# Kernel optimization log

Measured on AMD Instinct MI355X. Metric: run time of the kernel, lower is better.

The kernel has to match this reference:

```python
import jax, jax.numpy as jnp
import numpy as np

N, NFEAT, NHID, NHEADS, NCLASS = 8192, 512, 64, 8, 40
ALPHA = 0.2
NEG = jnp.float32(-9e15)


def _gat_layer(h, W, a, concat):
    # h: [N, Fin], W: [Fin, Fout], a: [2*Fout, 1]
    Fout = W.shape[1]
    Wh = h @ W                      # [N, Fout]
    f1 = Wh @ a[:Fout]              # [N, 1]
    f2 = Wh @ a[Fout:]              # [N, 1]
    e = jax.nn.leaky_relu(f1 + f2.T, negative_slope=ALPHA)  # [N, N]
    # NOTE: source masks on e > 0 (adj is NOT used) - replicate faithfully
    att = jax.nn.softmax(jnp.where(e > 0, e, NEG), axis=1)
    h_prime = att @ Wh              # [N, Fout]
    return jax.nn.elu(h_prime) if concat else h_prime


def setup_inputs() -> dict:
    key = jax.random.key(0)
    ks = jax.random.split(key, 6)
    x = jax.random.normal(ks[0], (N, NFEAT), dtype=jnp.float32)
    adj = jax.random.randint(ks[1], (N, N), 0, 2).astype(jnp.bool_)  # unused by math, kept for fidelity
    s = 0.1
    W_heads = jax.random.normal(ks[2], (NHEADS, NFEAT, NHID), dtype=jnp.float32) * s
    a_heads = jax.random.normal(ks[3], (NHEADS, 2 * NHID, 1), dtype=jnp.float32) * s
    W_out = jax.random.normal(ks[4], (NHID * NHEADS, NCLASS), dtype=jnp.float32) * s
    a_out = jax.random.normal(ks[5], (2 * NCLASS, 1), dtype=jnp.float32) * s
    return {"x": x, "adj": adj, "W_heads": W_heads, "a_heads": a_heads,
            "W_out": W_out, "a_out": a_out}


def reference(x, adj, W_heads, a_heads, W_out, a_out):
    # multi-head GAT layers (concat=True), vmapped over heads
    heads = jax.vmap(lambda W, a: _gat_layer(x, W, a, True))(W_heads, a_heads)  # [H, N, NHID]
    h = jnp.transpose(heads, (1, 0, 2)).reshape(N, NHEADS * NHID)
    # output attention layer (concat=False), then elu + log_softmax
    out = _gat_layer(h, W_out, a_out, False)
    out = jax.nn.elu(out)
    return jax.nn.log_softmax(out, axis=1)
```

## Files before the change

### kernel.cpp

```cpp
#include <hip/hip_runtime.h>
#include <math.h>

#define N_NODES 8192
#define NFEAT 512
#define NHID 64
#define NHEADS 8
#define NCLASS 40
#define NCHUNK 128
#define CHUNK 64
#define NB 4096

using bf16x8 = __attribute__((ext_vector_type(8))) short;
using f32x4 = __attribute__((ext_vector_type(4))) float;

__device__ __forceinline__ ushort f2b(float f) {
  uint u = __builtin_bit_cast(uint, f);
  u += 0x7FFFu + ((u >> 16) & 1u);
  return (ushort)(u >> 16);
}
__device__ __forceinline__ float b2f(ushort h) {
  uint u = (uint)h << 16;
  return __builtin_bit_cast(float, u);
}
__device__ __forceinline__ uint encf(float f) {
  uint u = __builtin_bit_cast(uint, f);
  return u ^ ((u >> 31) ? 0xFFFFFFFFu : 0x80000000u);
}
__device__ __forceinline__ float decf(uint u) {
  u ^= ((u >> 31) ? 0x80000000u : 0xFFFFFFFFu);
  return __builtin_bit_cast(float, u);
}
__device__ __forceinline__ float3 load_rng(const uint* mm, int head) {
  float h = decf(mm[head * 2]);
  float l = decf(~mm[head * 2 + 1]);
  float scale = (float)NB / fmaxf(h - l, 1e-30f);
  return make_float3(l, scale, h);
}
__device__ __forceinline__ int bucket_of(float v, float lo, float scale) {
  float u = fminf(fmaxf((v - lo) * scale, 0.f), (float)(NB - 1));
  return (int)u;
}

__global__ __launch_bounds__(256) void prep_k(const float* __restrict__ W_heads,
                                              ushort* __restrict__ bth,
                                              ushort* __restrict__ btl,
                                              float* __restrict__ zbase,
                                              int zcount) {
  int gid = blockIdx.x * 256 + threadIdx.x;
  int n = gid >> 9, c = gid & 511;
  int h = n >> 6, f = n & 63;
  float w = W_heads[((size_t)h * NFEAT + c) * NHID + f];
  ushort hh = f2b(w);
  bth[gid] = hh;
  btl[gid] = f2b(w - b2f(hh));
  if (gid < zcount) zbase[gid] = 0.f;
}

__global__ __launch_bounds__(256) void gemm1_k(const float* __restrict__ x,
                                               const ushort* __restrict__ bth,
                                               const ushort* __restrict__ btl,
                                               const float* __restrict__ a_heads,
                                               float* __restrict__ Wh,
                                               float* __restrict__ f1,
                                               float* __restrict__ f2,
                                               float* __restrict__ meanS,
                                               uint* __restrict__ mm1) {
  const int row0 = blockIdx.x * 128, col0 = blockIdx.y * 128;
  const int tid = threadIdx.x;
  const int wave = tid >> 6, lane = tid & 63;
  const int wr = wave >> 1, wc = wave & 1;
  __shared__ ushort Ah[128 * 40], Al[128 * 40], Bh[128 * 40], Bl[128 * 40];
  __shared__ float cs[2][64];
  __shared__ uint lmax[2], lmin[2];
  if (tid < 2) { lmax[tid] = 0u; lmin[tid] = 0u; }
  if (tid < 128) cs[tid >> 6][tid & 63] = 0.f;
  f32x4 acc[4][4] = {};
  const int sr = tid >> 1, sh = (tid & 1) * 16;
  const int fr = lane & 15, quad = lane >> 4;
  for (int k0 = 0; k0 < NFEAT; k0 += 32) {
    {
      const float* xs = x + (size_t)(row0 + sr) * NFEAT + k0 + sh;
      float av[16];
      *reinterpret_cast<float4*>(&av[0])  = *reinterpret_cast<const float4*>(xs);
      *reinterpret_cast<float4*>(&av[4])  = *reinterpret_cast<const float4*>(xs + 4);
      *reinterpret_cast<float4*>(&av[8])  = *reinterpret_cast<const float4*>(xs + 8);
      *reinterpret_cast<float4*>(&av[12]) = *reinterpret_cast<const float4*>(xs + 12);
      uint uh[8], ul[8];
#pragma unroll
      for (int q = 0; q < 8; ++q) {
        ushort h0 = f2b(av[2 * q]), h1 = f2b(av[2 * q + 1]);
        ushort l0 = f2b(av[2 * q] - b2f(h0)), l1 = f2b(av[2 * q + 1] - b2f(h1));
        uh[q] = (uint)h0 | ((uint)h1 << 16);
        ul[q] = (uint)l0 | ((uint)l1 << 16);
      }
      *reinterpret_cast<uint4*>(&Ah[sr * 40 + sh])     = make_uint4(uh[0], uh[1], uh[2], uh[3]);
      *reinterpret_cast<uint4*>(&Ah[sr * 40 + sh + 8]) = make_uint4(uh[4], uh[5], uh[6], uh[7]);
      *reinterpret_cast<uint4*>(&Al[sr * 40 + sh])     = make_uint4(ul[0], ul[1], ul[2], ul[3]);
      *reinterpret_cast<uint4*>(&Al[sr * 40 + sh + 8]) = make_uint4(ul[4], ul[5], ul[6], ul[7]);
      size_t boff = (size_t)(col0 + sr) * NFEAT + k0 + sh;
      *reinterpret_cast<uint4*>(&Bh[sr * 40 + sh])     = *reinterpret_cast<const uint4*>(bth + boff);
      *reinterpret_cast<uint4*>(&Bh[sr * 40 + sh + 8]) = *reinterpret_cast<const uint4*>(bth + boff + 8);
      *reinterpret_cast<uint4*>(&Bl[sr * 40 + sh])     = *reinterpret_cast<const uint4*>(btl + boff);
      *reinterpret_cast<uint4*>(&Bl[sr * 40 + sh + 8]) = *reinterpret_cast<const uint4*>(btl + boff + 8);
    }
    __syncthreads();
    bf16x8 afh[4], afl[4], bfh[4], bfl[4];
#pragma unroll
    for (int q = 0; q < 4; ++q) {
      afh[q] = *reinterpret_cast<const bf16x8*>(&Ah[(wr * 64 + q * 16 + fr) * 40 + quad * 8]);
      afl[q] = *reinterpret_cast<const bf16x8*>(&Al[(wr * 64 + q * 16 + fr) * 40 + quad * 8]);
      bfh[q] = *reinterpret_cast<const bf16x8*>(&Bh[(wc * 64 + q * 16 + fr) * 40 + quad * 8]);
      bfl[q] = *reinterpret_cast<const bf16x8*>(&Bl[(wc * 64 + q * 16 + fr) * 40 + quad * 8]);
    }
#pragma unroll
    for (int qr = 0; qr < 4; ++qr)
#pragma unroll
      for (int qc = 0; qc < 4; ++qc) {
        acc[qr][qc] = __builtin_amdgcn_mfma_f32_16x16x32_bf16(afl[qr], bfh[qc], acc[qr][qc], 0, 0, 0);
        acc[qr][qc] = __builtin_amdgcn_mfma_f32_16x16x32_bf16(afh[qr], bfl[qc], acc[qr][qc], 0, 0, 0);
        acc[qr][qc] = __builtin_amdgcn_mfma_f32_16x16x32_bf16(afh[qr], bfh[qc], acc[qr][qc], 0, 0, 0);
      }
    __syncthreads();
  }
  const int head = blockIdx.y * 2 + wc;
#pragma unroll
  for (int qr = 0; qr < 4; ++qr)
#pragma unroll
    for (int qc = 0; qc < 4; ++qc)
#pragma unroll
      for (int i = 0; i < 4; ++i) {
        int row = row0 + wr * 64 + qr * 16 + quad * 4 + i;
        int col = col0 + wc * 64 + qc * 16 + fr;
        Wh[(size_t)row * NFEAT + col] = acc[qr][qc][i];
      }
  const float* ah = a_heads + head * 2 * NHID;
  float a1v[4], a2v[4];
#pragma unroll
  for (int qc = 0; qc < 4; ++qc) { a1v[qc] = ah[qc * 16 + fr]; a2v[qc] = ah[NHID + qc * 16 + fr]; }
#pragma unroll
  for (int qr = 0; qr < 4; ++qr)
#pragma unroll
    for (int i = 0; i < 4; ++i) {
      float s1 = 0.f, s2 = 0.f;
#pragma unroll
      for (int qc = 0; qc < 4; ++qc) { s1 += acc[qr][qc][i] * a1v[qc]; s2 += acc[qr][qc][i] * a2v[qc]; }
#pragma unroll
      for (int m = 1; m < 16; m <<= 1) { s1 += __shfl_xor(s1, m, 64); s2 += __shfl_xor(s2, m, 64); }
      if (fr == 0) {
        int row = row0 + wr * 64 + qr * 16 + quad * 4 + i;
        f1[(head << 13) + row] = s1;
        f2[(head << 13) + row] = s2;
        atomicMax(&lmax[wc], encf(s2));
        atomicMax(&lmin[wc], ~encf(s2));
      }
    }
#pragma unroll
  for (int qc = 0; qc < 4; ++qc) {
    float v = 0.f;
#pragma unroll
    for (int qr = 0; qr < 4; ++qr)
#pragma unroll
      for (int i = 0; i < 4; ++i) v += acc[qr][qc][i];
    v += __shfl_xor(v, 16, 64);
    v += __shfl_xor(v, 32, 64);
    if (quad == 0) atomicAdd(&cs[wc][qc * 16 + fr], v);
  }
  __syncthreads();
  if (tid < 128) atomicAdd(&meanS[(blockIdx.y * 2 + (tid >> 6)) * NHID + (tid & 63)], cs[tid >> 6][tid & 63]);
  if (tid < 2) {
    atomicMax(&mm1[(blockIdx.y * 2 + tid) * 2], lmax[tid]);
    atomicMax(&mm1[(blockIdx.y * 2 + tid) * 2 + 1], lmin[tid]);
  }
}

__global__ __launch_bounds__(256) void gemm2_k(const float* __restrict__ H,
                                               const float* __restrict__ Wout,
                                               const float* __restrict__ a_out,
                                               float* __restrict__ Wh2,
                                               float* __restrict__ f1b,
                                               float* __restrict__ f2b,
                                               float* __restrict__ meanS2,
                                               uint* __restrict__ mm2) {
  const int row0 = blockIdx.x * 32;
  const int tid = threadIdx.x;
  __shared__ float As[32][33];
  __shared__ float Bs[32][40];
  __shared__ float cs[NCLASS];
  __shared__ uint lmax, lmin;
  if (tid < NCLASS) cs[tid] = 0.f;
  if (tid == 0) { lmax = 0u; lmin = 0u; }
  const int m = tid >> 3;
  const int n0 = (tid & 7) * 5;
  float acc[5] = {};
  for (int k0 = 0; k0 < NFEAT; k0 += 32) {
    {
      int kk = tid & 31, mq = tid >> 5;
#pragma unroll
      for (int r = 0; r < 4; ++r)
        As[kk][mq * 4 + r] = H[(size_t)(row0 + mq * 4 + r) * NFEAT + k0 + kk];
    }
    {
#pragma unroll
      for (int r = 0; r < 5; ++r) {
        int idx = tid + r * 256;
        if (idx < 1280) {
          int c = idx / 40, n = idx - c * 40;
          Bs[c][n] = Wout[(size_t)(k0 + c) * NCLASS + n];
        }
      }
    }
    __syncthreads();
#pragma unroll
    for (int kk = 0; kk < 32; ++kk) {
      float a = As[kk][m];
#pragma unroll
      for (int q = 0; q < 5; ++q) acc[q] += a * Bs[kk][n0 + q];
    }
    __syncthreads();
  }
#pragma unroll
  for (int q = 0; q < 5; ++q) Wh2[(size_t)(row0 + m) * NCLASS + n0 + q] = acc[q];
  float p1 = 0.f, p2 = 0.f;
#pragma unroll
  for (int q = 0; q < 5; ++q) {
    p1 += acc[q] * a_out[n0 + q];
    p2 += acc[q] * a_out[NCLASS + n0 + q];
  }
  p1 += __shfl_xor(p1, 1, 64); p1 += __shfl_xor(p1, 2, 64); p1 += __shfl_xor(p1, 4, 64);
  p2 += __shfl_xor(p2, 1, 64); p2 += __shfl_xor(p2, 2, 64); p2 += __shfl_xor(p2, 4, 64);
  if ((tid & 7) == 0) {
    f1b[row0 + m] = p1;
    f2b[row0 + m] = p2;
    atomicMax(&lmax, encf(p2));
    atomicMax(&lmin, ~encf(p2));
  }
#pragma unroll
  for (int q = 0; q < 5; ++q) atomicAdd(&cs[n0 + q], acc[q]);
  __syncthreads();
  if (tid < NCLASS) atomicAdd(&meanS2[tid], cs[tid]);
  if (tid == 0) { atomicMax(&mm2[0], lmax); atomicMax(&mm2[1], lmin); }
}

__global__ __launch_bounds__(1024) void bucket_k(const float* __restrict__ f2,
                                                 const uint* __restrict__ mm,
                                                 int* __restrict__ bs,
                                                 int* __restrict__ idxs,
                                                 float* __restrict__ f2s,
                                                 float* __restrict__ g) {
  __shared__ int sb[NB];
  const int head = blockIdx.x, tid = threadIdx.x;
  const int base = head * N_NODES;
  float3 rg = load_rng(mm, head);
#pragma unroll
  for (int r = 0; r < NB / 1024; ++r) sb[tid + r * 1024] = 0;
  __syncthreads();
  float v[8];
  int bk[8];
#pragma unroll
  for (int r = 0; r < 8; ++r) {
    v[r] = f2[base + tid + r * 1024];
    bk[r] = bucket_of(v[r], rg.x, rg.y);
    atomicAdd(&sb[bk[r]], 1);
  }
  __syncthreads();
  for (int st = 1; st < NB; st <<= 1) {
    int t[NB / 1024];
#pragma unroll
    for (int r = 0; r < NB / 1024; ++r) { int i = tid + r * 1024; t[r] = (i >= st) ? sb[i - st] : 0; }
    __syncthreads();
#pragma unroll
    for (int r = 0; r < NB / 1024; ++r) sb[tid + r * 1024] += t[r];
    __syncthreads();
  }
  int ex[NB / 1024];
#pragma unroll
  for (int r = 0; r < NB / 1024; ++r) {
    int b = tid + r * 1024;
    ex[r] = b ? sb[b - 1] : 0;
    bs[head * (NB + 1) + b] = ex[r];
  }
  if (tid == 0) bs[head * (NB + 1) + NB] = sb[NB - 1];
  __syncthreads();
#pragma unroll
  for (int r = 0; r < NB / 1024; ++r) sb[tid + r * 1024] = ex[r];
  __syncthreads();
#pragma unroll
  for (int r = 0; r < 8; ++r) {
    int pos = atomicAdd(&sb[bk[r]], 1);
    int i = tid + r * 1024;
    idxs[base + pos] = i;
    f2s[base + pos] = v[r];
    g[base + pos] = expf(v[r] - rg.z);
  }
}

template <int F, int LD, int COLSTEP>
__global__ __launch_bounds__(256) void scanA_k(const float* __restrict__ Wh,
                                               const float* __restrict__ g,
                                               const int* __restrict__ idxs,
                                               float* __restrict__ S,
                                               float* __restrict__ D,
                                               float* __restrict__ T_,
                                               float* __restrict__ Td) {
  constexpr int PAD = (F == 64) ? 66 : 42;
  const int head = blockIdx.y, chunk = blockIdx.x;
  const int tid = threadIdx.x, w = tid >> 6, lane = tid & 63;
  const int base = head << 13;
  const int kbase = base + chunk * CHUNK;
  __shared__ float Sloc[64][PAD];
  __shared__ float Dloc[64];
  __shared__ float wtot[4][PAD];
  __shared__ float wtotD[4];
  int myj = 0; float myg = 0.f;
  if (lane < 16) {
    myj = idxs[kbase + w * 16 + lane];
    myg = g[kbase + w * 16 + lane];
  }
  float acc = 0.f, accD = 0.f;
#pragma unroll
  for (int kk = 15; kk >= 0; --kk) {
    int j = __shfl(myj, kk, 64);
    float gk = __shfl(myg, kk, 64);
    float wv = (lane < F) ? Wh[(size_t)j * LD + head * COLSTEP + lane] : 0.f;
    acc += gk * wv;
    accD += gk;
    if (lane < F) Sloc[w * 16 + kk][lane] = acc;
    if (lane == 0) Dloc[w * 16 + kk] = accD;
  }
  if (lane < F) wtot[w][lane] = acc;
  if (lane == 0) wtotD[w] = accD;
  __syncthreads();
  float off = 0.f, offD = 0.f;
#pragma unroll
  for (int w2 = 1; w2 < 4; ++w2) {
    if (w + w2 < 4) {
      off += (lane < F) ? wtot[w + w2][lane] : 0.f;
      offD += wtotD[w + w2];
    }
  }
#pragma unroll
  for (int kk = 0; kk < 16; ++kk) {
    int e = w * 16 + kk;
    if (lane < F) S[(size_t)(kbase + e) * F + lane] = Sloc[e][lane] + off;
    if (lane == 0) D[kbase + e] = Dloc[e] + offD;
  }
  if (w == 0) {
    if (lane < F) T_[(size_t)(head * NCHUNK + chunk) * F + lane] = wtot[0][lane] + off;
    if (lane == 0) Td[head * NCHUNK + chunk] = wtotD[0] + offD;
  }
}

template <int F>
__global__ __launch_bounds__(1024) void scanB_k(float* __restrict__ T_, float* __restrict__ Td) {
  __shared__ float s[NCHUNK * F];
  __shared__ float td[NCHUNK];
  int head = blockIdx.x;
  int tid = threadIdx.x, slot = tid >> 6, lane = tid & 63;
#pragma unroll
  for (int r = 0; r < 8; ++r) {
    int c = r * 16 + slot;
    if (lane < F) s[c * F + lane] = T_[(size_t)(head * NCHUNK + c) * F + lane];
  }
  if (tid < NCHUNK) td[tid] = Td[head * NCHUNK + tid];
  __syncthreads();
  for (int st = 1; st < NCHUNK; st <<= 1) {
    float v[8];
    float tv = 0.f;
#pragma unroll
    for (int r = 0; r < 8; ++r) {
      int c = r * 16 + slot;
      v[r] = (lane < F && c + st < NCHUNK) ? s[(c + st) * F + lane] : 0.f;
    }
    if (tid < NCHUNK && tid + st < NCHUNK) tv = td[tid + st];
    __syncthreads();
#pragma unroll
    for (int r = 0; r < 8; ++r) {
      int c = r * 16 + slot;
      if (lane < F) s[c * F + lane] += v[r];
    }
    if (tid < NCHUNK) td[tid] += tv;
    __syncthreads();
  }
#pragma unroll
  for (int r = 0; r < 8; ++r) {
    int c = r * 16 + slot;
    if (lane < F) T_[(size_t)(head * NCHUNK + c) * F + lane] = s[c * F + lane];
  }
  if (tid < NCHUNK) Td[head * NCHUNK + tid] = td[tid];
}

__global__ __launch_bounds__(256) void query1_k(const float* __restrict__ f1,
                                                const float* __restrict__ f2s,
                                                const int* __restrict__ idxs,
                                                const float* __restrict__ Wh,
                                                const float* __restrict__ S,
                                                const float* __restrict__ D,
                                                const float* __restrict__ T_,
                                                const float* __restrict__ Td,
                                                const uint* __restrict__ mm,
                                                const int* __restrict__ bs,
                                                const float* __restrict__ meanS,
                                                float* __restrict__ H) {
  int w = blockIdx.x * 4 + (threadIdx.x >> 6);
  int lane = threadIdx.x & 63;
  int head = w & 7, i = w >> 3, base = head << 13;
  float t = f1[base + i];
  float3 rg = load_rng(mm, head);
  int B0 = bucket_of(-t, rg.x, rg.y);
  int p0 = bs[head * (NB + 1) + B0], p1 = bs[head * (NB + 1) + B0 + 1];
  float num = 0.f, den = 0.f;
  int cnt = N_NODES - p1;
  if (p1 < N_NODES) {
    int c = p1 >> 6;
    num = S[(size_t)(base + p1) * NHID + lane] +
          ((c + 1 < NCHUNK) ? T_[(size_t)(head * NCHUNK + c + 1) * NHID + lane] : 0.f);
    den = D[base + p1] + ((c + 1 < NCHUNK) ? Td[head * NCHUNK + c + 1] : 0.f);
  }
  for (int p = p0; p < p1; ++p) {
    float v = f2s[base + p];
    if (t + v > 0.f) {
      int j = idxs[base + p];
      float gk = expf(v - rg.z);
      num += gk * Wh[(size_t)j * NFEAT + head * NHID + lane];
      den += gk;
      ++cnt;
    }
  }
  float val = cnt ? num / den : meanS[head * NHID + lane] * (1.f / N_NODES);
  H[(size_t)i * NFEAT + head * NHID + lane] = (val > 0.f) ? val : expm1f(val);
}

__global__ __launch_bounds__(256) void final_k(const float* __restrict__ f1b,
                                               const float* __restrict__ f2bs,
                                               const int* __restrict__ idx2,
                                               const float* __restrict__ Wh2,
                                               const float* __restrict__ S2,
                                               const float* __restrict__ D2,
                                               const float* __restrict__ T2,
                                               const float* __restrict__ Td2,
                                               const uint* __restrict__ mm2,
                                               const int* __restrict__ bs2,
                                               const float* __restrict__ meanS2,
                                               float* __restrict__ out) {
  int i = blockIdx.x * 4 + (threadIdx.x >> 6);
  int lane = threadIdx.x & 63;
  float t = f1b[i];
  float3 rg = load_rng(mm2, 0);
  int B0 = bucket_of(-t, rg.x, rg.y);
  int p0 = bs2[B0], p1 = bs2[B0 + 1];
  float num = 0.f, den = 0.f;
  int cnt = N_NODES - p1;
  if (p1 < N_NODES) {
    int c = p1 >> 6;
    num = (lane < NCLASS) ? (S2[(size_t)p1 * NCLASS + lane] +
                             ((c + 1 < NCHUNK) ? T2[(size_t)(c + 1) * NCLASS + lane] : 0.f))
                          : 0.f;
    den = D2[p1] + ((c + 1 < NCHUNK) ? Td2[c + 1] : 0.f);
  }
  for (int p = p0; p < p1; ++p) {
    float v = f2bs[p];
    if (t + v > 0.f) {
      int j = idx2[p];
      float gk = expf(v - rg.z);
      if (lane < NCLASS) num += gk * Wh2[(size_t)j * NCLASS + lane];
      den += gk;
      ++cnt;
    }
  }
  float o;
  if (lane < NCLASS) {
    float val = cnt ? num / den : meanS2[lane] * (1.f / N_NODES);
    o = (val > 0.f) ? val : expm1f(val);
  } else {
    o = -INFINITY;
  }
  float m = o;
#pragma unroll
  for (int msk = 32; msk; msk >>= 1) m = fmaxf(m, __shfl_xor(m, msk, 64));
  float e = (lane < NCLASS) ? expf(o - m) : 0.f;
#pragma unroll
  for (int msk = 32; msk; msk >>= 1) e += __shfl_xor(e, msk, 64);
  if (lane < NCLASS) out[(size_t)i * NCLASS + lane] = o - m - logf(e);
}

extern "C" void kernel_launch(void* const* d_in, const int* in_sizes, int n_in,
                              void* d_out, int out_size, void* d_ws, size_t ws_size,
                              hipStream_t stream) {
  const float* x       = (const float*)d_in[0];
  const float* W_heads = (const float*)d_in[2];
  const float* a_heads = (const float*)d_in[3];
  const float* W_out   = (const float*)d_in[4];
  const float* a_out   = (const float*)d_in[5];
  float* out = (float*)d_out;

  float* ws = (float*)d_ws;
  size_t o = 0;
  auto alloc = [&](size_t n) { float* p = ws + o; o += (n + 3) & ~(size_t)3; return p; };
  float*  S1     = alloc((size_t)NHEADS * N_NODES * NHID);
  ushort* BTh    = (ushort*)alloc((size_t)NFEAT * NFEAT / 2);
  ushort* BTl    = (ushort*)alloc((size_t)NFEAT * NFEAT / 2);
  float*  Wh     = alloc((size_t)N_NODES * NFEAT);
  float*  H      = alloc((size_t)N_NODES * NFEAT);
  float*  f1     = alloc(NHEADS * N_NODES);
  float*  f2     = alloc(NHEADS * N_NODES);
  float*  f2s    = alloc(NHEADS * N_NODES);
  int*    idxs   = (int*)alloc(NHEADS * N_NODES);
  float*  g1     = alloc(NHEADS * N_NODES);
  float*  D1     = alloc(NHEADS * N_NODES);
  float*  T1     = alloc(NHEADS * NCHUNK * NHID);
  float*  Td1    = alloc(NHEADS * NCHUNK);
  int*    bst1   = (int*)alloc(NHEADS * (NB + 1));
  float*  Wh2    = alloc((size_t)N_NODES * NCLASS);
  float*  S2     = alloc((size_t)N_NODES * NCLASS);
  float*  f1b    = alloc(N_NODES);
  float*  f2b    = alloc(N_NODES);
  float*  f2bs   = alloc(N_NODES);
  int*    idx2   = (int*)alloc(N_NODES);
  float*  g2     = alloc(N_NODES);
  float*  D2     = alloc(N_NODES);
  float*  T2     = alloc(NCHUNK * NCLASS);
  float*  Td2    = alloc(NCHUNK);
  int*    bst2   = (int*)alloc(NB + 1);
  float*  zbase  = ws + o;
  uint*   mm1    = (uint*)alloc(16);
  uint*   mm2    = (uint*)alloc(4);
  float*  meanS1 = alloc(NHEADS * NHID);
  float*  meanS2 = alloc(64);
  int zcount = (int)((ws + o) - zbase);

  prep_k<<<1024, 256, 0, stream>>>(W_heads, BTh, BTl, zbase, zcount);
  gemm1_k<<<dim3(64, 4), 256, 0, stream>>>(x, BTh, BTl, a_heads, Wh, f1, f2, meanS1, mm1);
  bucket_k<<<NHEADS, 1024, 0, stream>>>(f2, mm1, bst1, idxs, f2s, g1);
  scanA_k<NHID, NFEAT, NHID><<<dim3(NCHUNK, NHEADS), 256, 0, stream>>>(Wh, g1, idxs, S1, D1, T1, Td1);
  scanB_k<NHID><<<NHEADS, 1024, 0, stream>>>(T1, Td1);
  query1_k<<<16384, 256, 0, stream>>>(f1, f2s, idxs, Wh, S1, D1, T1, Td1, mm1, bst1, meanS1, H);

  gemm2_k<<<256, 256, 0, stream>>>(H, W_out, a_out, Wh2, f1b, f2b, meanS2, mm2);
  bucket_k<<<1, 1024, 0, stream>>>(f2b, mm2, bst2, idx2, f2bs, g2);
  scanA_k<NCLASS, NCLASS, 0><<<dim3(NCHUNK, 1), 256, 0, stream>>>(Wh2, g2, idx2, S2, D2, T2, Td2);
  scanB_k<NCLASS><<<1, 1024, 0, stream>>>(T2, Td2);
  final_k<<<2048, 256, 0, stream>>>(f1b, f2bs, idx2, Wh2, S2, D2, T2, Td2, mm2, bst2, meanS2, out);
}
```

Before: 536.7 us.

## Double-buffer gemm1 tiles, swap grid order, and move gemm2 to split-bf16 MFMA

```diff
diff --git a/kernel.cpp b/kernel.cpp
--- a/kernel.cpp
+++ b/kernel.cpp
@@ -42,18 +42,31 @@
 }
 
 __global__ __launch_bounds__(256) void prep_k(const float* __restrict__ W_heads,
+                                              const float* __restrict__ Wout,
                                               ushort* __restrict__ bth,
                                               ushort* __restrict__ btl,
+                                              ushort* __restrict__ bt2h,
+                                              ushort* __restrict__ bt2l,
                                               float* __restrict__ zbase,
                                               int zcount) {
-  int gid = blockIdx.x * 256 + threadIdx.x;
-  int n = gid >> 9, c = gid & 511;
-  int h = n >> 6, f = n & 63;
-  float w = W_heads[((size_t)h * NFEAT + c) * NHID + f];
-  ushort hh = f2b(w);
-  bth[gid] = hh;
-  btl[gid] = f2b(w - b2f(hh));
-  if (gid < zcount) zbase[gid] = 0.f;
+  int b = blockIdx.x, t = threadIdx.x;
+  if (b < 1024) {
+    int gid = b * 256 + t;
+    int n = gid >> 9, c = gid & 511;
+    int h = n >> 6, f = n & 63;
+    float w = W_heads[((size_t)h * NFEAT + c) * NHID + f];
+    ushort hh = f2b(w);
+    bth[gid] = hh;
+    btl[gid] = f2b(w - b2f(hh));
+    if (gid < zcount) zbase[gid] = 0.f;
+  } else {
+    int gid = (b - 1024) * 256 + t;
+    int n = gid >> 9, c = gid & 511;
+    float w = (n < NCLASS) ? Wout[(size_t)c * NCLASS + n] : 0.f;
+    ushort hh = f2b(w);
+    bt2h[gid] = hh;
+    bt2l[gid] = f2b(w - b2f(hh));
+  }
 }
 
 __global__ __launch_bounds__(256) void gemm1_k(const float* __restrict__ x,
@@ -65,11 +78,11 @@
                                                float* __restrict__ f2,
                                                float* __restrict__ meanS,
                                                uint* __restrict__ mm1) {
-  const int row0 = blockIdx.x * 128, col0 = blockIdx.y * 128;
+  const int col0 = blockIdx.x * 128, row0 = blockIdx.y * 128;
   const int tid = threadIdx.x;
   const int wave = tid >> 6, lane = tid & 63;
   const int wr = wave >> 1, wc = wave & 1;
-  __shared__ ushort Ah[128 * 40], Al[128 * 40], Bh[128 * 40], Bl[128 * 40];
+  __shared__ ushort Ah[2][128 * 40], Al[2][128 * 40], Bh[2][128 * 40], Bl[2][128 * 40];
   __shared__ float cs[2][64];
   __shared__ uint lmax[2], lmin[2];
   if (tid < 2) { lmax[tid] = 0u; lmin[tid] = 0u; }
@@ -77,40 +90,53 @@
   f32x4 acc[4][4] = {};
   const int sr = tid >> 1, sh = (tid & 1) * 16;
   const int fr = lane & 15, quad = lane >> 4;
-  for (int k0 = 0; k0 < NFEAT; k0 += 32) {
-    {
-      const float* xs = x + (size_t)(row0 + sr) * NFEAT + k0 + sh;
-      float av[16];
-      *reinterpret_cast<float4*>(&av[0])  = *reinterpret_cast<const float4*>(xs);
-      *reinterpret_cast<float4*>(&av[4])  = *reinterpret_cast<const float4*>(xs + 4);
-      *reinterpret_cast<float4*>(&av[8])  = *reinterpret_cast<const float4*>(xs + 8);
-      *reinterpret_cast<float4*>(&av[12]) = *reinterpret_cast<const float4*>(xs + 12);
-      uint uh[8], ul[8];
-#pragma unroll
-      for (int q = 0; q < 8; ++q) {
-        ushort h0 = f2b(av[2 * q]), h1 = f2b(av[2 * q + 1]);
-        ushort l0 = f2b(av[2 * q] - b2f(h0)), l1 = f2b(av[2 * q + 1] - b2f(h1));
-        uh[q] = (uint)h0 | ((uint)h1 << 16);
-        ul[q] = (uint)l0 | ((uint)l1 << 16);
-      }
-      *reinterpret_cast<uint4*>(&Ah[sr * 40 + sh])     = make_uint4(uh[0], uh[1], uh[2], uh[3]);
-      *reinterpret_cast<uint4*>(&Ah[sr * 40 + sh + 8]) = make_uint4(uh[4], uh[5], uh[6], uh[7]);
-      *reinterpret_cast<uint4*>(&Al[sr * 40 + sh])     = make_uint4(ul[0], ul[1], ul[2], ul[3]);
-      *reinterpret_cast<uint4*>(&Al[sr * 40 + sh + 8]) = make_uint4(ul[4], ul[5], ul[6], ul[7]);
-      size_t boff = (size_t)(col0 + sr) * NFEAT + k0 + sh;
-      *reinterpret_cast<uint4*>(&Bh[sr * 40 + sh])     = *reinterpret_cast<const uint4*>(bth + boff);
-      *reinterpret_cast<uint4*>(&Bh[sr * 40 + sh + 8]) = *reinterpret_cast<const uint4*>(bth + boff + 8);
-      *reinterpret_cast<uint4*>(&Bl[sr * 40 + sh])     = *reinterpret_cast<const uint4*>(btl + boff);
-      *reinterpret_cast<uint4*>(&Bl[sr * 40 + sh + 8]) = *reinterpret_cast<const uint4*>(btl + boff + 8);
-    }
+
+  float av[16];
+  uint4 bh0, bh1, bl0, bl1;
+  auto load_tile = [&](int k0) {
+    const float* xs = x + (size_t)(row0 + sr) * NFEAT + k0 + sh;
+    *reinterpret_cast<float4*>(&av[0])  = *reinterpret_cast<const float4*>(xs);
+    *reinterpret_cast<float4*>(&av[4])  = *reinterpret_cast<const float4*>(xs + 4);
+    *reinterpret_cast<float4*>(&av[8])  = *reinterpret_cast<const float4*>(xs + 8);
+    *reinterpret_cast<float4*>(&av[12]) = *reinterpret_cast<const float4*>(xs + 12);
+    size_t boff = (size_t)(col0 + sr) * NFEAT + k0 + sh;
+    bh0 = *reinterpret_cast<const uint4*>(bth + boff);
+    bh1 = *reinterpret_cast<const uint4*>(bth + boff + 8);
+    bl0 = *reinterpret_cast<const uint4*>(btl + boff);
+    bl1 = *reinterpret_cast<const uint4*>(btl + boff + 8);
+  };
+  auto store_tile = [&](int buf) {
+    uint uh[8], ul[8];
+#pragma unroll
+    for (int q = 0; q < 8; ++q) {
+      ushort h0 = f2b(av[2 * q]), h1 = f2b(av[2 * q + 1]);
+      ushort l0 = f2b(av[2 * q] - b2f(h0)), l1 = f2b(av[2 * q + 1] - b2f(h1));
+      uh[q] = (uint)h0 | ((uint)h1 << 16);
+      ul[q] = (uint)l0 | ((uint)l1 << 16);
+    }
+    *reinterpret_cast<uint4*>(&Ah[buf][sr * 40 + sh])     = make_uint4(uh[0], uh[1], uh[2], uh[3]);
+    *reinterpret_cast<uint4*>(&Ah[buf][sr * 40 + sh + 8]) = make_uint4(uh[4], uh[5], uh[6], uh[7]);
+    *reinterpret_cast<uint4*>(&Al[buf][sr * 40 + sh])     = make_uint4(ul[0], ul[1], ul[2], ul[3]);
+    *reinterpret_cast<uint4*>(&Al[buf][sr * 40 + sh + 8]) = make_uint4(ul[4], ul[5], ul[6], ul[7]);
+    *reinterpret_cast<uint4*>(&Bh[buf][sr * 40 + sh])     = bh0;
+    *reinterpret_cast<uint4*>(&Bh[buf][sr * 40 + sh + 8]) = bh1;
+    *reinterpret_cast<uint4*>(&Bl[buf][sr * 40 + sh])     = bl0;
+    *reinterpret_cast<uint4*>(&Bl[buf][sr * 40 + sh + 8]) = bl1;
+  };
+
+  load_tile(0);
+  store_tile(0);
+  for (int it = 0; it < 16; ++it) {
+    const int buf = it & 1;
+    if (it < 15) load_tile((it + 1) * 32);
     __syncthreads();
     bf16x8 afh[4], afl[4], bfh[4], bfl[4];
 #pragma unroll
     for (int q = 0; q < 4; ++q) {
-      afh[q] = *reinterpret_cast<const bf16x8*>(&Ah[(wr * 64 + q * 16 + fr) * 40 + quad * 8]);
-      afl[q] = *reinterpret_cast<const bf16x8*>(&Al[(wr * 64 + q * 16 + fr) * 40 + quad * 8]);
-      bfh[q] = *reinterpret_cast<const bf16x8*>(&Bh[(wc * 64 + q * 16 + fr) * 40 + quad * 8]);
-      bfl[q] = *reinterpret_cast<const bf16x8*>(&Bl[(wc * 64 + q * 16 + fr) * 40 + quad * 8]);
+      afh[q] = *reinterpret_cast<const bf16x8*>(&Ah[buf][(wr * 64 + q * 16 + fr) * 40 + quad * 8]);
+      afl[q] = *reinterpret_cast<const bf16x8*>(&Al[buf][(wr * 64 + q * 16 + fr) * 40 + quad * 8]);
+      bfh[q] = *reinterpret_cast<const bf16x8*>(&Bh[buf][(wc * 64 + q * 16 + fr) * 40 + quad * 8]);
+      bfl[q] = *reinterpret_cast<const bf16x8*>(&Bl[buf][(wc * 64 + q * 16 + fr) * 40 + quad * 8]);
     }
 #pragma unroll
     for (int qr = 0; qr < 4; ++qr)
@@ -120,9 +146,9 @@
         acc[qr][qc] = __builtin_amdgcn_mfma_f32_16x16x32_bf16(afh[qr], bfl[qc], acc[qr][qc], 0, 0, 0);
         acc[qr][qc] = __builtin_amdgcn_mfma_f32_16x16x32_bf16(afh[qr], bfh[qc], acc[qr][qc], 0, 0, 0);
       }
-    __syncthreads();
-  }
-  const int head = blockIdx.y * 2 + wc;
+    if (it < 15) store_tile(buf ^ 1);
+  }
+  const int head = blockIdx.x * 2 + wc;
 #pragma unroll
   for (int qr = 0; qr < 4; ++qr)
 #pragma unroll
@@ -166,76 +192,126 @@
     if (quad == 0) atomicAdd(&cs[wc][qc * 16 + fr], v);
   }
   __syncthreads();
-  if (tid < 128) atomicAdd(&meanS[(blockIdx.y * 2 + (tid >> 6)) * NHID + (tid & 63)], cs[tid >> 6][tid & 63]);
+  if (tid < 128) atomicAdd(&meanS[(blockIdx.x * 2 + (tid >> 6)) * NHID + (tid & 63)], cs[tid >> 6][tid & 63]);
   if (tid < 2) {
-    atomicMax(&mm1[(blockIdx.y * 2 + tid) * 2], lmax[tid]);
-    atomicMax(&mm1[(blockIdx.y * 2 + tid) * 2 + 1], lmin[tid]);
+    atomicMax(&mm1[(blockIdx.x * 2 + tid) * 2], lmax[tid]);
+    atomicMax(&mm1[(blockIdx.x * 2 + tid) * 2 + 1], lmin[tid]);
   }
 }
 
 __global__ __launch_bounds__(256) void gemm2_k(const float* __restrict__ H,
-                                               const float* __restrict__ Wout,
+                                               const ushort* __restrict__ bt2h,
+                                               const ushort* __restrict__ bt2l,
                                                const float* __restrict__ a_out,
                                                float* __restrict__ Wh2,
-                                               float* __restrict__ f1b,
-                                               float* __restrict__ f2b,
+                                               float* __restrict__ f1bv,
+                                               float* __restrict__ f2bv,
                                                float* __restrict__ meanS2,
                                                uint* __restrict__ mm2) {
-  const int row0 = blockIdx.x * 32;
+  const int row0 = blockIdx.x * 128;
   const int tid = threadIdx.x;
-  __shared__ float As[32][33];
-  __shared__ float Bs[32][40];
-  __shared__ float cs[NCLASS];
+  const int w = tid >> 6, lane = tid & 63;
+  const int fr = lane & 15, quad = lane >> 4;
+  __shared__ ushort Ah[128 * 40], Al[128 * 40];
+  __shared__ ushort Bh[48 * 40], Bl[48 * 40];
+  __shared__ float cs[48];
   __shared__ uint lmax, lmin;
-  if (tid < NCLASS) cs[tid] = 0.f;
+  if (tid < 48) cs[tid] = 0.f;
   if (tid == 0) { lmax = 0u; lmin = 0u; }
-  const int m = tid >> 3;
-  const int n0 = (tid & 7) * 5;
-  float acc[5] = {};
+  f32x4 acc[2][3] = {};
+  const int sr = tid >> 1, sh = (tid & 1) * 16;
   for (int k0 = 0; k0 < NFEAT; k0 += 32) {
     {
-      int kk = tid & 31, mq = tid >> 5;
-#pragma unroll
-      for (int r = 0; r < 4; ++r)
-        As[kk][mq * 4 + r] = H[(size_t)(row0 + mq * 4 + r) * NFEAT + k0 + kk];
-    }
-    {
-#pragma unroll
-      for (int r = 0; r < 5; ++r) {
-        int idx = tid + r * 256;
-        if (idx < 1280) {
-          int c = idx / 40, n = idx - c * 40;
-          Bs[c][n] = Wout[(size_t)(k0 + c) * NCLASS + n];
-        }
+      const float* hs = H + (size_t)(row0 + sr) * NFEAT + k0 + sh;
+      float av[16];
+      *reinterpret_cast<float4*>(&av[0])  = *reinterpret_cast<const float4*>(hs);
+      *reinterpret_cast<float4*>(&av[4])  = *reinterpret_cast<const float4*>(hs + 4);
+      *reinterpret_cast<float4*>(&av[8])  = *reinterpret_cast<const float4*>(hs + 8);
+      *reinterpret_cast<float4*>(&av[12]) = *reinterpret_cast<const float4*>(hs + 12);
+      uint uh[8], ul[8];
+#pragma unroll
+      for (int q = 0; q < 8; ++q) {
+        ushort h0 = f2b(av[2 * q]), h1 = f2b(av[2 * q + 1]);
+        ushort l0 = f2b(av[2 * q] - b2f(h0)), l1 = f2b(av[2 * q + 1] - b2f(h1));
+        uh[q] = (uint)h0 | ((uint)h1 << 16);
+        ul[q] = (uint)l0 | ((uint)l1 << 16);
+      }
+      *reinterpret_cast<uint4*>(&Ah[sr * 40 + sh])     = make_uint4(uh[0], uh[1], uh[2], uh[3]);
+      *reinterpret_cast<uint4*>(&Ah[sr * 40 + sh + 8]) = make_uint4(uh[4], uh[5], uh[6], uh[7]);
+      *reinterpret_cast<uint4*>(&Al[sr * 40 + sh])     = make_uint4(ul[0], ul[1], ul[2], ul[3]);
+      *reinterpret_cast<uint4*>(&Al[sr * 40 + sh + 8]) = make_uint4(ul[4], ul[5], ul[6], ul[7]);
+      if (tid < 96) {
+        int n = tid >> 1, h2 = (tid & 1) * 16;
+        size_t boff = (size_t)n * NFEAT + k0 + h2;
+        *reinterpret_cast<uint4*>(&Bh[n * 40 + h2])     = *reinterpret_cast<const uint4*>(bt2h + boff);
+        *reinterpret_cast<uint4*>(&Bh[n * 40 + h2 + 8]) = *reinterpret_cast<const uint4*>(bt2h + boff + 8);
+        *reinterpret_cast<uint4*>(&Bl[n * 40 + h2])     = *reinterpret_cast<const uint4*>(bt2l + boff);
+        *reinterpret_cast<uint4*>(&Bl[n * 40 + h2 + 8]) = *reinterpret_cast<const uint4*>(bt2l + boff + 8);
       }
     }
     __syncthreads();
-#pragma unroll
-    for (int kk = 0; kk < 32; ++kk) {
-      float a = As[kk][m];
-#pragma unroll
-      for (int q = 0; q < 5; ++q) acc[q] += a * Bs[kk][n0 + q];
-    }
+    bf16x8 afh[2], afl[2], bfh[3], bfl[3];
+#pragma unroll
+    for (int rt = 0; rt < 2; ++rt) {
+      afh[rt] = *reinterpret_cast<const bf16x8*>(&Ah[(w * 32 + rt * 16 + fr) * 40 + quad * 8]);
+      afl[rt] = *reinterpret_cast<const bf16x8*>(&Al[(w * 32 + rt * 16 + fr) * 40 + quad * 8]);
+    }
+#pragma unroll
+    for (int ct = 0; ct < 3; ++ct) {
+      bfh[ct] = *reinterpret_cast<const bf16x8*>(&Bh[(ct * 16 + fr) * 40 + quad * 8]);
+      bfl[ct] = *reinterpret_cast<const bf16x8*>(&Bl[(ct * 16 + fr) * 40 + quad * 8]);
+    }
+#pragma unroll
+    for (int rt = 0; rt < 2; ++rt)
+#pragma unroll
+      for (int ct = 0; ct < 3; ++ct) {
+        acc[rt][ct] = __builtin_amdgcn_mfma_f32_16x16x32_bf16(afl[rt], bfh[ct], acc[rt][ct], 0, 0, 0);
+        acc[rt][ct] = __builtin_amdgcn_mfma_f32_16x16x32_bf16(afh[rt], bfl[ct], acc[rt][ct], 0, 0, 0);
+        acc[rt][ct] = __builtin_amdgcn_mfma_f32_16x16x32_bf16(afh[rt], bfh[ct], acc[rt][ct], 0, 0, 0);
+      }
     __syncthreads();
   }
-#pragma unroll
-  for (int q = 0; q < 5; ++q) Wh2[(size_t)(row0 + m) * NCLASS + n0 + q] = acc[q];
-  float p1 = 0.f, p2 = 0.f;
-#pragma unroll
-  for (int q = 0; q < 5; ++q) {
-    p1 += acc[q] * a_out[n0 + q];
-    p2 += acc[q] * a_out[NCLASS + n0 + q];
-  }
-  p1 += __shfl_xor(p1, 1, 64); p1 += __shfl_xor(p1, 2, 64); p1 += __shfl_xor(p1, 4, 64);
-  p2 += __shfl_xor(p2, 1, 64); p2 += __shfl_xor(p2, 2, 64); p2 += __shfl_xor(p2, 4, 64);
-  if ((tid & 7) == 0) {
-    f1b[row0 + m] = p1;
-    f2b[row0 + m] = p2;
-    atomicMax(&lmax, encf(p2));
-    atomicMax(&lmin, ~encf(p2));
-  }
-#pragma unroll
-  for (int q = 0; q < 5; ++q) atomicAdd(&cs[n0 + q], acc[q]);
+  float a1v[3], a2v[3];
+#pragma unroll
+  for (int ct = 0; ct < 3; ++ct) {
+    int col = ct * 16 + fr;
+    a1v[ct] = (col < NCLASS) ? a_out[col] : 0.f;
+    a2v[ct] = (col < NCLASS) ? a_out[NCLASS + col] : 0.f;
+  }
+#pragma unroll
+  for (int rt = 0; rt < 2; ++rt)
+#pragma unroll
+    for (int i = 0; i < 4; ++i) {
+      int row = row0 + w * 32 + rt * 16 + quad * 4 + i;
+      float s1 = 0.f, s2 = 0.f;
+#pragma unroll
+      for (int ct = 0; ct < 3; ++ct) {
+        int col = ct * 16 + fr;
+        float v = acc[rt][ct][i];
+        if (col < NCLASS) Wh2[(size_t)row * NCLASS + col] = v;
+        s1 += v * a1v[ct];
+        s2 += v * a2v[ct];
+      }
+#pragma unroll
+      for (int m = 1; m < 16; m <<= 1) { s1 += __shfl_xor(s1, m, 64); s2 += __shfl_xor(s2, m, 64); }
+      if (fr == 0) {
+        f1bv[row] = s1;
+        f2bv[row] = s2;
+        atomicMax(&lmax, encf(s2));
+        atomicMax(&lmin, ~encf(s2));
+      }
+    }
+#pragma unroll
+  for (int ct = 0; ct < 3; ++ct) {
+    float v = 0.f;
+#pragma unroll
+    for (int rt = 0; rt < 2; ++rt)
+#pragma unroll
+      for (int i = 0; i < 4; ++i) v += acc[rt][ct][i];
+    v += __shfl_xor(v, 16, 64);
+    v += __shfl_xor(v, 32, 64);
+    if (quad == 0) atomicAdd(&cs[ct * 16 + fr], v);
+  }
   __syncthreads();
   if (tid < NCLASS) atomicAdd(&meanS2[tid], cs[tid]);
   if (tid == 0) { atomicMax(&mm2[0], lmax); atomicMax(&mm2[1], lmin); }
@@ -499,6 +575,8 @@
   float*  S1     = alloc((size_t)NHEADS * N_NODES * NHID);
   ushort* BTh    = (ushort*)alloc((size_t)NFEAT * NFEAT / 2);
   ushort* BTl    = (ushort*)alloc((size_t)NFEAT * NFEAT / 2);
+  ushort* BT2h   = (ushort*)alloc((size_t)48 * NFEAT / 2);
+  ushort* BT2l   = (ushort*)alloc((size_t)48 * NFEAT / 2);
   float*  Wh     = alloc((size_t)N_NODES * NFEAT);
   float*  H      = alloc((size_t)N_NODES * NFEAT);
   float*  f1     = alloc(NHEADS * N_NODES);
@@ -528,14 +606,14 @@
   float*  meanS2 = alloc(64);
   int zcount = (int)((ws + o) - zbase);
 
-  prep_k<<<1024, 256, 0, stream>>>(W_heads, BTh, BTl, zbase, zcount);
-  gemm1_k<<<dim3(64, 4), 256, 0, stream>>>(x, BTh, BTl, a_heads, Wh, f1, f2, meanS1, mm1);
+  prep_k<<<1024 + 96, 256, 0, stream>>>(W_heads, W_out, BTh, BTl, BT2h, BT2l, zbase, zcount);
+  gemm1_k<<<dim3(4, 64), 256, 0, stream>>>(x, BTh, BTl, a_heads, Wh, f1, f2, meanS1, mm1);
   bucket_k<<<NHEADS, 1024, 0, stream>>>(f2, mm1, bst1, idxs, f2s, g1);
   scanA_k<NHID, NFEAT, NHID><<<dim3(NCHUNK, NHEADS), 256, 0, stream>>>(Wh, g1, idxs, S1, D1, T1, Td1);
   scanB_k<NHID><<<NHEADS, 1024, 0, stream>>>(T1, Td1);
   query1_k<<<16384, 256, 0, stream>>>(f1, f2s, idxs, Wh, S1, D1, T1, Td1, mm1, bst1, meanS1, H);
 
-  gemm2_k<<<256, 256, 0, stream>>>(H, W_out, a_out, Wh2, f1b, f2b, meanS2, mm2);
+  gemm2_k<<<64, 256, 0, stream>>>(H, BT2h, BT2l, a_out, Wh2, f1b, f2b, meanS2, mm2);
   bucket_k<<<1, 1024, 0, stream>>>(f2b, mm2, bst2, idx2, f2bs, g2);
   scanA_k<NCLASS, NCLASS, 0><<<dim3(NCHUNK, 1), 256, 0, stream>>>(Wh2, g2, idx2, S2, D2, T2, Td2);
   scanB_k<NCLASS><<<1, 1024, 0, stream>>>(T2, Td2);
```

Result: faster. 498.6 us, median of 2 (-7.1%).
